# Optimization experiments

Hardware: AMD Instinct MI355X
Metric: run time of the kernel (lower is better)

The kernel has to match this reference:

```python
import jax, jax.numpy as jnp
import numpy as np

N_NODES = 100000
D_IN = 128
D_OUT = 128
N_EDGES = 50000
EDGE_SIZE = 16  # nodes per hyperedge (assumed unique within an edge)


def setup_inputs() -> dict:
    key = jax.random.key(0)
    ks = jax.random.split(key, 8)
    # hypergraph in flat membership (CSR-like) form
    member_nodes = jax.random.randint(ks[0], (N_EDGES * EDGE_SIZE,), 0, N_NODES)
    edge_ids = jnp.repeat(jnp.arange(N_EDGES), EDGE_SIZE)
    H = jax.random.normal(ks[1], (N_NODES, D_IN), dtype=jnp.float32)
    input_weight = jax.random.uniform(ks[2], (N_NODES, 2), dtype=jnp.float32)
    std = 1.0 / np.sqrt(D_OUT)
    W = jax.random.uniform(ks[3], (D_IN, D_OUT), minval=-std, maxval=std, dtype=jnp.float32)
    bias = jax.random.uniform(ks[4], (D_OUT,), minval=-std, maxval=std, dtype=jnp.float32)

    def lin(k, fan_in, fan_out):
        b = 1.0 / np.sqrt(fan_in)
        k1, k2 = jax.random.split(k)
        w = jax.random.uniform(k1, (fan_in, fan_out), minval=-b, maxval=b, dtype=jnp.float32)
        bb = jax.random.uniform(k2, (fan_out,), minval=-b, maxval=b, dtype=jnp.float32)
        return w, bb

    fc1_w, fc1_b = lin(ks[5], 2, 10)
    fc2_w, fc2_b = lin(ks[6], 10, 5)
    fc3_w, fc3_b = lin(ks[7], 5, 1)
    return {
        "member_nodes": member_nodes, "edge_ids": edge_ids,
        "H": H, "input_weight": input_weight,
        "W": W, "bias": bias,
        "fc1_w": fc1_w, "fc1_b": fc1_b,
        "fc2_w": fc2_w, "fc2_b": fc2_b,
        "fc3_w": fc3_w, "fc3_b": fc3_b,
    }


def reference(member_nodes, edge_ids, H, input_weight, W, bias,
              fc1_w, fc1_b, fc2_w, fc2_b, fc3_w, fc3_b):
    # Weight_net (eval mode -> dropout is identity): per-node scalar weight in (0,1)
    h1 = jax.nn.relu(input_weight @ fc1_w + fc1_b)
    h2 = jax.nn.relu(h1 @ fc2_w + fc2_b)
    W2 = jax.nn.sigmoid(h2 @ fc3_w + fc3_b)  # [N, 1]

    # signal_shift_hypergraph_: per-edge weighted sum, broadcast, scatter-add
    HW2 = H * W2                                   # [N, d]
    gathered = HW2[member_nodes]                   # [M, d]
    edge_sum = jax.ops.segment_sum(gathered, edge_ids, num_segments=N_EDGES)   # [E, d]
    edge_size = jax.ops.segment_sum(jnp.ones((member_nodes.shape[0],), H.dtype),
                                    edge_ids, num_segments=N_EDGES)            # [E]
    contrib = (edge_sum[edge_ids] - H[member_nodes]) / (edge_size[edge_ids] - 1.0)[:, None]
    new_signal = H + jax.ops.segment_sum(contrib, member_nodes, num_segments=N_NODES)

    # row-normalize (1/rowsum with inf -> 0)
    rowsum = new_signal.sum(axis=1)
    r_inv = jnp.where(rowsum != 0, 1.0 / rowsum, 0.0)
    AH = new_signal * r_inv[:, None]

    return AH @ W + bias
```

## Files before the change

### kernel.cpp

```cpp
#include <hip/hip_runtime.h>
#include <math.h>

#define EDGE_SZ 16
#define CAP 32
#define BIN_CAP 2560

typedef __attribute__((ext_vector_type(8))) short bf16x8;
typedef __attribute__((ext_vector_type(4))) float f32x4;

__device__ __forceinline__ unsigned short f2bf(float x) {
    unsigned u = __builtin_bit_cast(unsigned, x);
    unsigned r = (u + 0x7fff + ((u >> 16) & 1)) >> 16;
    return (unsigned short)r;
}
__device__ __forceinline__ unsigned pack2bf(float lo, float hi) {
    return ((unsigned)f2bf(hi) << 16) | (unsigned)f2bf(lo);
}
__device__ __forceinline__ float bf_lo(unsigned u) {
    return __builtin_bit_cast(float, u << 16);
}
__device__ __forceinline__ float bf_hi(unsigned u) {
    return __builtin_bit_cast(float, u & 0xffff0000u);
}

__global__ __launch_bounds__(256) void init_kernel(
    const float* __restrict__ W, unsigned short* __restrict__ Wtg,
    int* __restrict__ binCursor, int nbins,
    unsigned* __restrict__ esbSent, float* __restrict__ SeSent)
{
    int i = blockIdx.x * blockDim.x + threadIdx.x;
    if (i < nbins) binCursor[i] = 0;
    if (i < 64) esbSent[i] = 0u;
    if (i == 64) *SeSent = 0.f;
    if (i < 16384) {
        int nn = i >> 7, k = i & 127;
        Wtg[i] = f2bf(W[k * 128 + nn]);
    }
}

__global__ __launch_bounds__(256) void bin_kernel(
    const int* __restrict__ mn, int* __restrict__ binCursor,
    unsigned* __restrict__ stage, int m)
{
    __shared__ int hist[512];
    __shared__ int base[512];
    int t = threadIdx.x;
    for (int i = t; i < 512; i += 256) hist[i] = 0;
    __syncthreads();
    int start = blockIdx.x * 2048;
    int nodev[8], loff[8];
#pragma unroll
    for (int j = 0; j < 8; ++j) {
        int i = start + j * 256 + t;
        nodev[j] = (i < m) ? mn[i] : -1;
        loff[j] = (nodev[j] >= 0) ? atomicAdd(&hist[nodev[j] >> 8], 1) : 0;
    }
    __syncthreads();
    for (int b = t; b < 512; b += 256)
        base[b] = (hist[b] > 0) ? atomicAdd(&binCursor[b], hist[b]) : 0;
    __syncthreads();
#pragma unroll
    for (int j = 0; j < 8; ++j) {
        if (nodev[j] >= 0) {
            int b = nodev[j] >> 8;
            int pos = base[b] + loff[j];
            int i = start + j * 256 + t;
            if (pos < BIN_CAP)
                stage[b * BIN_CAP + pos] =
                    ((unsigned)(i >> 4) << 8) | (unsigned)(nodev[j] & 255);
        }
    }
}

__global__ __launch_bounds__(256) void bucket_prep_kernel(
    const unsigned* __restrict__ stage, const int* __restrict__ binCursor,
    unsigned short* __restrict__ bucket, int* __restrict__ cursor,
    const float* __restrict__ H, const float* __restrict__ iw,
    const float* __restrict__ fc1_w, const float* __restrict__ fc1_b,
    const float* __restrict__ fc2_w, const float* __restrict__ fc2_b,
    const float* __restrict__ fc3_w, const float* __restrict__ fc3_b,
    unsigned* __restrict__ Hwb, float* __restrict__ Hs, float* __restrict__ Hws,
    int n, int nbins, int E)
{
    __shared__ __align__(16) unsigned short lb[256 * CAP];
    __shared__ int lc[256];
    int t = threadIdx.x;
    if ((int)blockIdx.x < nbins) {
        int b = blockIdx.x;
        unsigned sent = (unsigned)E * 0x10001u;
        for (int i = t; i < 4096; i += 256) ((unsigned*)lb)[i] = sent;
        lc[t] = 0;
        __syncthreads();
        int cnt = binCursor[b]; if (cnt > BIN_CAP) cnt = BIN_CAP;
        for (int i = t; i < cnt; i += 256) {
            unsigned u = stage[b * BIN_CAP + i];
            int nloc = u & 255;
            int e = u >> 8;
            int p = atomicAdd(&lc[nloc], 1);
            if (p < CAP) lb[nloc * CAP + p] = (unsigned short)e;
        }
        __syncthreads();
        int nbase = b << 8;
        for (int i = t; i < 1024; i += 256) {
            int nloc = i >> 2;
            int node = nbase + nloc;
            if (node < n)
                ((uint4*)bucket)[(size_t)node * 4 + (i & 3)] = ((const uint4*)lb)[i];
        }
        int node = nbase + t;
        if (node < n) cursor[node] = lc[t];
        return;
    }
    int wave = __builtin_amdgcn_readfirstlane(
        ((int)blockIdx.x - nbins) * (blockDim.x >> 6) + (t >> 6));
    int lane = t & 63;
    if (wave >= n) return;
    float xx = iw[wave * 2 + 0], xy = iw[wave * 2 + 1];
    float h1[10];
#pragma unroll
    for (int j = 0; j < 10; ++j) {
        float v = xx * fc1_w[j] + xy * fc1_w[10 + j] + fc1_b[j];
        h1[j] = v > 0.f ? v : 0.f;
    }
    float h2[5];
#pragma unroll
    for (int j = 0; j < 5; ++j) {
        float v = fc2_b[j];
#pragma unroll
        for (int k = 0; k < 10; ++k) v += h1[k] * fc2_w[k * 5 + j];
        h2[j] = v > 0.f ? v : 0.f;
    }
    float z = fc3_b[0];
#pragma unroll
    for (int j = 0; j < 5; ++j) z += h2[j] * fc3_w[j];
    float w2v = 1.f / (1.f + expf(-z));

    float2 h = ((const float2*)H)[wave * 64 + lane];
    Hwb[wave * 64 + lane] = pack2bf(h.x * w2v, h.y * w2v);
    float part = h.x + h.y;
#pragma unroll
    for (int off = 32; off >= 1; off >>= 1) part += __shfl_xor(part, off, 64);
    if (lane == 0) { Hs[wave] = part; Hws[wave] = part * w2v; }
}

__global__ __launch_bounds__(256) void edge_sum_kernel(
    const int* __restrict__ mn, const unsigned* __restrict__ Hwb,
    const float* __restrict__ Hws, unsigned* __restrict__ esb,
    float* __restrict__ Se, int E)
{
    int pair = __builtin_amdgcn_readfirstlane(
        blockIdx.x * (blockDim.x >> 6) + (threadIdx.x >> 6));
    int lane = threadIdx.x & 63;
    int e0 = pair * 2;
    if (e0 >= E) return;
    int e1 = e0 + 1;
    int n0[EDGE_SZ], n1[EDGE_SZ];
#pragma unroll
    for (int m = 0; m < EDGE_SZ; ++m) n0[m] = mn[e0 * EDGE_SZ + m];
#pragma unroll
    for (int m = 0; m < EDGE_SZ; ++m) n1[m] = mn[e1 * EDGE_SZ + m];
    unsigned u0[EDGE_SZ], u1[EDGE_SZ];
#pragma unroll
    for (int m = 0; m < EDGE_SZ; ++m) u0[m] = Hwb[n0[m] * 64 + lane];
#pragma unroll
    for (int m = 0; m < EDGE_SZ; ++m) u1[m] = Hwb[n1[m] * 64 + lane];
    float se0 = 0.f, se1 = 0.f;
#pragma unroll
    for (int m = 0; m < EDGE_SZ; ++m) { se0 += Hws[n0[m]]; se1 += Hws[n1[m]]; }
    float ax0 = 0.f, ay0 = 0.f, ax1 = 0.f, ay1 = 0.f;
#pragma unroll
    for (int m = 0; m < EDGE_SZ; ++m) {
        ax0 += bf_lo(u0[m]); ay0 += bf_hi(u0[m]);
        ax1 += bf_lo(u1[m]); ay1 += bf_hi(u1[m]);
    }
    esb[e0 * 64 + lane] = pack2bf(ax0, ay0);
    esb[e1 * 64 + lane] = pack2bf(ax1, ay1);
    if (lane == 0) { Se[e0] = se0; Se[e1] = se1; }
}

__global__ __launch_bounds__(256) void node_update_kernel(
    const float* __restrict__ H, const unsigned* __restrict__ esb,
    const float* __restrict__ Hs, const float* __restrict__ Se,
    const int* __restrict__ cursor, const unsigned short* __restrict__ bucket,
    unsigned* __restrict__ AHb, int n, int E)
{
    int grp = __builtin_amdgcn_readfirstlane(
        blockIdx.x * (blockDim.x >> 6) + (threadIdx.x >> 6));
    int lane = threadIdx.x & 63;
    int base = grp * 4;
    if (base >= n) return;
    float2 h[4];
    int d[4];
    const unsigned* bp[4];
    float ax[4], ay[4], ss[4];
    int dm = 0;
#pragma unroll
    for (int q = 0; q < 4; ++q) {
        int nq = base + q; if (nq >= n) nq = n - 1;
        h[q] = ((const float2*)H)[nq * 64 + lane];
        int dq = cursor[nq]; if (dq > CAP) dq = CAP;
        if (base + q >= n) dq = 0;
        d[q] = dq;
        if (dq > dm) dm = dq;
        bp[q] = (const unsigned*)(bucket + (size_t)nq * CAP);
        ax[q] = 0.f; ay[q] = 0.f; ss[q] = 0.f;
    }
    for (int k0 = 0; k0 < dm; k0 += 8) {
        unsigned ev[4][8];
#pragma unroll
        for (int q = 0; q < 4; ++q)
#pragma unroll
            for (int j = 0; j < 8; ++j) {
                unsigned dw = bp[q][(k0 >> 1) + (j >> 1)];
                ev[q][j] = (j & 1) ? (dw >> 16) : (dw & 0xffffu);
            }
        unsigned v[4][8];
#pragma unroll
        for (int q = 0; q < 4; ++q)
#pragma unroll
            for (int j = 0; j < 8; ++j) v[q][j] = esb[ev[q][j] * 64 + lane];
        float s[4][8];
#pragma unroll
        for (int q = 0; q < 4; ++q)
#pragma unroll
            for (int j = 0; j < 8; ++j) s[q][j] = Se[ev[q][j]];
#pragma unroll
        for (int q = 0; q < 4; ++q)
#pragma unroll
            for (int j = 0; j < 8; ++j) {
                ax[q] += bf_lo(v[q][j]);
                ay[q] += bf_hi(v[q][j]);
                ss[q] += s[q][j];
            }
    }
    const float inv15 = 1.f / 15.f;
#pragma unroll
    for (int q = 0; q < 4; ++q) {
        if (base + q >= n) break;
        int nq = base + q;
        float sc = 1.f - (float)d[q] * inv15;
        float nx = h[q].x * sc + ax[q] * inv15;
        float ny = h[q].y * sc + ay[q] * inv15;
        float st = Hs[nq] * sc + ss[q] * inv15;
        float ri = (st != 0.f) ? 1.f / st : 0.f;
        AHb[nq * 64 + lane] = pack2bf(nx * ri, ny * ri);
    }
}

#define WT_LD 136
__global__ __launch_bounds__(256) void gemm_kernel(
    const unsigned short* __restrict__ AHb, const unsigned short* __restrict__ Wtg,
    const float* __restrict__ bias, float* __restrict__ out, int M)
{
    __shared__ short Wt[128 * WT_LD];
    int t = threadIdx.x;
    for (int i = t; i < 8192; i += 256) {
        unsigned dw = ((const unsigned*)Wtg)[i];
        int n = i >> 6, k2 = i & 63;
        *(unsigned*)&Wt[n * WT_LD + k2 * 2] = dw;
    }
    __syncthreads();

    int lane = t & 63;
    int m16 = lane & 15;
    int quad = lane >> 4;
    int wrow0 = blockIdx.x * 64 + (t >> 6) * 16;

    int arow = wrow0 + m16;
    if (arow >= M) arow = M - 1;

    f32x4 acc[8] = {};
#pragma unroll
    for (int kc = 0; kc < 4; ++kc) {
        int k0 = kc * 32;
        bf16x8 a = *(const bf16x8*)&AHb[arow * 128 + k0 + quad * 8];
#pragma unroll
        for (int ct = 0; ct < 8; ++ct) {
            bf16x8 b = *(const bf16x8*)&Wt[(ct * 16 + m16) * WT_LD + k0 + quad * 8];
            acc[ct] = __builtin_amdgcn_mfma_f32_16x16x32_bf16(a, b, acc[ct], 0, 0, 0);
        }
    }

#pragma unroll
    for (int ct = 0; ct < 8; ++ct) {
        float bv = bias[ct * 16 + m16];
#pragma unroll
        for (int r = 0; r < 4; ++r) {
            int row = wrow0 + quad * 4 + r;
            if (row < M)
                out[row * 128 + ct * 16 + m16] = acc[ct][r] + bv;
        }
    }
}

extern "C" void kernel_launch(void* const* d_in, const int* in_sizes, int n_in,
                              void* d_out, int out_size, void* d_ws, size_t ws_size,
                              hipStream_t stream)
{
    const int*   mn   = (const int*)d_in[0];
    const float* H    = (const float*)d_in[2];
    const float* iw   = (const float*)d_in[3];
    const float* W    = (const float*)d_in[4];
    const float* bias = (const float*)d_in[5];
    const float* fc1w = (const float*)d_in[6];
    const float* fc1b = (const float*)d_in[7];
    const float* fc2w = (const float*)d_in[8];
    const float* fc2b = (const float*)d_in[9];
    const float* fc3w = (const float*)d_in[10];
    const float* fc3b = (const float*)d_in[11];
    float* out = (float*)d_out;

    const int M = in_sizes[0];
    const int E = M / EDGE_SZ;
    const int N = in_sizes[2] / 128;
    const int nbins = (N + 255) >> 8;

    char* ws = (char*)d_ws;
    size_t off = 0;
    auto alloc = [&](size_t bytes) -> char* {
        char* p = ws + off;
        off = (off + bytes + 15) & ~(size_t)15;
        return p;
    };
    unsigned*       Hwb    = (unsigned*)alloc((size_t)N * 64 * 4);
    float*          Hs     = (float*)alloc((size_t)N * 4);
    float*          Hws    = (float*)alloc((size_t)N * 4);
    unsigned*       esb    = (unsigned*)alloc((size_t)(E + 1) * 64 * 4);
    float*          Se     = (float*)alloc((size_t)(E + 1) * 4);
    unsigned*       AHb    = (unsigned*)alloc((size_t)N * 64 * 4);
    int*            cursor = (int*)alloc((size_t)N * 4);
    unsigned short* bucket = (unsigned short*)alloc((size_t)N * CAP * 2);
    unsigned short* Wtg    = (unsigned short*)alloc((size_t)128 * 128 * 2);
    int*            binCur = (int*)alloc((size_t)nbins * 4);
    unsigned*       stage  = (unsigned*)alloc((size_t)nbins * BIN_CAP * 4);
    (void)ws_size;

    const int prep_blocks = (N + 3) / 4;

    init_kernel<<<64, 256, 0, stream>>>(W, Wtg, binCur, nbins,
                                        esb + (size_t)E * 64, Se + E);
    bin_kernel<<<(M + 2047) / 2048, 256, 0, stream>>>(mn, binCur, stage, M);
    bucket_prep_kernel<<<nbins + prep_blocks, 256, 0, stream>>>(
        stage, binCur, bucket, cursor,
        H, iw, fc1w, fc1b, fc2w, fc2b, fc3w, fc3b, Hwb, Hs, Hws, N, nbins, E);
    edge_sum_kernel<<<(E / 2 + 3) / 4, 256, 0, stream>>>(mn, Hwb, Hws, esb, Se, E);
    node_update_kernel<<<((N + 3) / 4 + 3) / 4, 256, 0, stream>>>(
        H, esb, Hs, Se, cursor, bucket, AHb, N, E);
    gemm_kernel<<<(N + 63) / 64, 256, 0, stream>>>(
        (const unsigned short*)AHb, Wtg, bias, out, N);
}
```

Before: 249.3 us.

## Regroup pipeline stages to co-launch binning with prep and bucketing with edge sums

The binning pass now shares one launch with the per-node weight-net/prep work, and the bucket build shares one launch with the edge-sum work. Each pairing combines independent stages as disjoint block ranges of one grid, so there is one fewer kernel launch and the independent pieces can overlap on the GPU. The trade-off is that the bucketing blocks, with their large shared-memory footprint, now run alongside the edge-sum waves and may lower occupancy for those waves.

```diff
diff --git a/kernel.cpp b/kernel.cpp
--- a/kernel.cpp
+++ b/kernel.cpp
@@ -38,49 +38,85 @@
     }
 }
 
-__global__ __launch_bounds__(256) void bin_kernel(
+__global__ __launch_bounds__(256) void bin_prep_kernel(
     const int* __restrict__ mn, int* __restrict__ binCursor,
-    unsigned* __restrict__ stage, int m)
-{
-    __shared__ int hist[512];
-    __shared__ int base[512];
-    int t = threadIdx.x;
-    for (int i = t; i < 512; i += 256) hist[i] = 0;
-    __syncthreads();
-    int start = blockIdx.x * 2048;
-    int nodev[8], loff[8];
-#pragma unroll
-    for (int j = 0; j < 8; ++j) {
-        int i = start + j * 256 + t;
-        nodev[j] = (i < m) ? mn[i] : -1;
-        loff[j] = (nodev[j] >= 0) ? atomicAdd(&hist[nodev[j] >> 8], 1) : 0;
-    }
-    __syncthreads();
-    for (int b = t; b < 512; b += 256)
-        base[b] = (hist[b] > 0) ? atomicAdd(&binCursor[b], hist[b]) : 0;
-    __syncthreads();
-#pragma unroll
-    for (int j = 0; j < 8; ++j) {
-        if (nodev[j] >= 0) {
-            int b = nodev[j] >> 8;
-            int pos = base[b] + loff[j];
-            int i = start + j * 256 + t;
-            if (pos < BIN_CAP)
-                stage[b * BIN_CAP + pos] =
-                    ((unsigned)(i >> 4) << 8) | (unsigned)(nodev[j] & 255);
-        }
-    }
-}
-
-__global__ __launch_bounds__(256) void bucket_prep_kernel(
-    const unsigned* __restrict__ stage, const int* __restrict__ binCursor,
-    unsigned short* __restrict__ bucket, int* __restrict__ cursor,
+    unsigned* __restrict__ stage, int m,
     const float* __restrict__ H, const float* __restrict__ iw,
     const float* __restrict__ fc1_w, const float* __restrict__ fc1_b,
     const float* __restrict__ fc2_w, const float* __restrict__ fc2_b,
     const float* __restrict__ fc3_w, const float* __restrict__ fc3_b,
     unsigned* __restrict__ Hwb, float* __restrict__ Hs, float* __restrict__ Hws,
-    int n, int nbins, int E)
+    int n, int bin_blocks)
+{
+    __shared__ int hist[512];
+    __shared__ int base[512];
+    int t = threadIdx.x;
+    if ((int)blockIdx.x < bin_blocks) {
+        for (int i = t; i < 512; i += 256) hist[i] = 0;
+        __syncthreads();
+        int start = blockIdx.x * 2048;
+        int nodev[8], loff[8];
+#pragma unroll
+        for (int j = 0; j < 8; ++j) {
+            int i = start + j * 256 + t;
+            nodev[j] = (i < m) ? mn[i] : -1;
+            loff[j] = (nodev[j] >= 0) ? atomicAdd(&hist[nodev[j] >> 8], 1) : 0;
+        }
+        __syncthreads();
+        for (int b = t; b < 512; b += 256)
+            base[b] = (hist[b] > 0) ? atomicAdd(&binCursor[b], hist[b]) : 0;
+        __syncthreads();
+#pragma unroll
+        for (int j = 0; j < 8; ++j) {
+            if (nodev[j] >= 0) {
+                int b = nodev[j] >> 8;
+                int pos = base[b] + loff[j];
+                int i = start + j * 256 + t;
+                if (pos < BIN_CAP)
+                    stage[b * BIN_CAP + pos] =
+                        ((unsigned)(i >> 4) << 8) | (unsigned)(nodev[j] & 255);
+            }
+        }
+        return;
+    }
+    int wave = __builtin_amdgcn_readfirstlane(
+        ((int)blockIdx.x - bin_blocks) * (blockDim.x >> 6) + (t >> 6));
+    int lane = t & 63;
+    if (wave >= n) return;
+    float xx = iw[wave * 2 + 0], xy = iw[wave * 2 + 1];
+    float h1[10];
+#pragma unroll
+    for (int j = 0; j < 10; ++j) {
+        float v = xx * fc1_w[j] + xy * fc1_w[10 + j] + fc1_b[j];
+        h1[j] = v > 0.f ? v : 0.f;
+    }
+    float h2[5];
+#pragma unroll
+    for (int j = 0; j < 5; ++j) {
+        float v = fc2_b[j];
+#pragma unroll
+        for (int k = 0; k < 10; ++k) v += h1[k] * fc2_w[k * 5 + j];
+        h2[j] = v > 0.f ? v : 0.f;
+    }
+    float z = fc3_b[0];
+#pragma unroll
+    for (int j = 0; j < 5; ++j) z += h2[j] * fc3_w[j];
+    float w2v = 1.f / (1.f + expf(-z));
+
+    float2 h = ((const float2*)H)[wave * 64 + lane];
+    Hwb[wave * 64 + lane] = pack2bf(h.x * w2v, h.y * w2v);
+    float part = h.x + h.y;
+#pragma unroll
+    for (int off = 32; off >= 1; off >>= 1) part += __shfl_xor(part, off, 64);
+    if (lane == 0) { Hs[wave] = part; Hws[wave] = part * w2v; }
+}
+
+__global__ __launch_bounds__(256) void bucket_edge_kernel(
+    const unsigned* __restrict__ stage, const int* __restrict__ binCursor,
+    unsigned short* __restrict__ bucket, int* __restrict__ cursor,
+    const int* __restrict__ mn, const unsigned* __restrict__ Hwb,
+    const float* __restrict__ Hws, unsigned* __restrict__ esb,
+    float* __restrict__ Se, int n, int nbins, int E)
 {
     __shared__ __align__(16) unsigned short lb[256 * CAP];
     __shared__ int lc[256];
@@ -111,67 +147,30 @@
         if (node < n) cursor[node] = lc[t];
         return;
     }
-    int wave = __builtin_amdgcn_readfirstlane(
+    int pair = __builtin_amdgcn_readfirstlane(
         ((int)blockIdx.x - nbins) * (blockDim.x >> 6) + (t >> 6));
     int lane = t & 63;
-    if (wave >= n) return;
-    float xx = iw[wave * 2 + 0], xy = iw[wave * 2 + 1];
-    float h1[10];
-#pragma unroll
-    for (int j = 0; j < 10; ++j) {
-        float v = xx * fc1_w[j] + xy * fc1_w[10 + j] + fc1_b[j];
-        h1[j] = v > 0.f ? v : 0.f;
-    }
-    float h2[5];
-#pragma unroll
-    for (int j = 0; j < 5; ++j) {
-        float v = fc2_b[j];
-#pragma unroll
-        for (int k = 0; k < 10; ++k) v += h1[k] * fc2_w[k * 5 + j];
-        h2[j] = v > 0.f ? v : 0.f;
-    }
-    float z = fc3_b[0];
-#pragma unroll
-    for (int j = 0; j < 5; ++j) z += h2[j] * fc3_w[j];
-    float w2v = 1.f / (1.f + expf(-z));
-
-    float2 h = ((const float2*)H)[wave * 64 + lane];
-    Hwb[wave * 64 + lane] = pack2bf(h.x * w2v, h.y * w2v);
-    float part = h.x + h.y;
-#pragma unroll
-    for (int off = 32; off >= 1; off >>= 1) part += __shfl_xor(part, off, 64);
-    if (lane == 0) { Hs[wave] = part; Hws[wave] = part * w2v; }
-}
-
-__global__ __launch_bounds__(256) void edge_sum_kernel(
-    const int* __restrict__ mn, const unsigned* __restrict__ Hwb,
-    const float* __restrict__ Hws, unsigned* __restrict__ esb,
-    float* __restrict__ Se, int E)
-{
-    int pair = __builtin_amdgcn_readfirstlane(
-        blockIdx.x * (blockDim.x >> 6) + (threadIdx.x >> 6));
-    int lane = threadIdx.x & 63;
     int e0 = pair * 2;
     if (e0 >= E) return;
     int e1 = e0 + 1;
     int n0[EDGE_SZ], n1[EDGE_SZ];
 #pragma unroll
-    for (int m = 0; m < EDGE_SZ; ++m) n0[m] = mn[e0 * EDGE_SZ + m];
-#pragma unroll
-    for (int m = 0; m < EDGE_SZ; ++m) n1[m] = mn[e1 * EDGE_SZ + m];
+    for (int mm = 0; mm < EDGE_SZ; ++mm) n0[mm] = mn[e0 * EDGE_SZ + mm];
+#pragma unroll
+    for (int mm = 0; mm < EDGE_SZ; ++mm) n1[mm] = mn[e1 * EDGE_SZ + mm];
     unsigned u0[EDGE_SZ], u1[EDGE_SZ];
 #pragma unroll
-    for (int m = 0; m < EDGE_SZ; ++m) u0[m] = Hwb[n0[m] * 64 + lane];
-#pragma unroll
-    for (int m = 0; m < EDGE_SZ; ++m) u1[m] = Hwb[n1[m] * 64 + lane];
+    for (int mm = 0; mm < EDGE_SZ; ++mm) u0[mm] = Hwb[n0[mm] * 64 + lane];
+#pragma unroll
+    for (int mm = 0; mm < EDGE_SZ; ++mm) u1[mm] = Hwb[n1[mm] * 64 + lane];
     float se0 = 0.f, se1 = 0.f;
 #pragma unroll
-    for (int m = 0; m < EDGE_SZ; ++m) { se0 += Hws[n0[m]]; se1 += Hws[n1[m]]; }
+    for (int mm = 0; mm < EDGE_SZ; ++mm) { se0 += Hws[n0[mm]]; se1 += Hws[n1[mm]]; }
     float ax0 = 0.f, ay0 = 0.f, ax1 = 0.f, ay1 = 0.f;
 #pragma unroll
-    for (int m = 0; m < EDGE_SZ; ++m) {
-        ax0 += bf_lo(u0[m]); ay0 += bf_hi(u0[m]);
-        ax1 += bf_lo(u1[m]); ay1 += bf_hi(u1[m]);
+    for (int mm = 0; mm < EDGE_SZ; ++mm) {
+        ax0 += bf_lo(u0[mm]); ay0 += bf_hi(u0[mm]);
+        ax1 += bf_lo(u1[mm]); ay1 += bf_hi(u1[mm]);
     }
     esb[e0 * 64 + lane] = pack2bf(ax0, ay0);
     esb[e1 * 64 + lane] = pack2bf(ax1, ay1);
@@ -335,15 +334,17 @@
     unsigned*       stage  = (unsigned*)alloc((size_t)nbins * BIN_CAP * 4);
     (void)ws_size;
 
+    const int bin_blocks  = (M + 2047) / 2048;
     const int prep_blocks = (N + 3) / 4;
+    const int edge_blocks = (E / 2 + 3) / 4;
 
     init_kernel<<<64, 256, 0, stream>>>(W, Wtg, binCur, nbins,
                                         esb + (size_t)E * 64, Se + E);
-    bin_kernel<<<(M + 2047) / 2048, 256, 0, stream>>>(mn, binCur, stage, M);
-    bucket_prep_kernel<<<nbins + prep_blocks, 256, 0, stream>>>(
-        stage, binCur, bucket, cursor,
-        H, iw, fc1w, fc1b, fc2w, fc2b, fc3w, fc3b, Hwb, Hs, Hws, N, nbins, E);
-    edge_sum_kernel<<<(E / 2 + 3) / 4, 256, 0, stream>>>(mn, Hwb, Hws, esb, Se, E);
+    bin_prep_kernel<<<bin_blocks + prep_blocks, 256, 0, stream>>>(
+        mn, binCur, stage, M,
+        H, iw, fc1w, fc1b, fc2w, fc2b, fc3w, fc3b, Hwb, Hs, Hws, N, bin_blocks);
+    bucket_edge_kernel<<<nbins + edge_blocks, 256, 0, stream>>>(
+        stage, binCur, bucket, cursor, mn, Hwb, Hws, esb, Se, N, nbins, E);
     node_update_kernel<<<((N + 3) / 4 + 3) / 4, 256, 0, stream>>>(
         H, esb, Hs, Se, cursor, bucket, AHb, N, E);
     gemm_kernel<<<(N + 63) / 64, 256, 0, stream>>>(
```

Result: no change. 247.2 us (-0.8%).
